# Optimization experiments

Hardware: AMD Instinct MI355X
Metric: run time of the kernel (lower is better)

The kernel has to match this reference:

```python
import jax, jax.numpy as jnp
import numpy as np

V, D, S, H, B = 32000, 1024, 2048, 16, 4
DFF = 4 * D
HD = D // H
EPS = 1e-5


def _layernorm(x, g, b):
    mu = jnp.mean(x, axis=-1, keepdims=True)
    var = jnp.var(x, axis=-1, keepdims=True)
    return (x - mu) * jax.lax.rsqrt(var + EPS) * g + b


def setup_inputs() -> dict:
    key = jax.random.key(0)
    ks = jax.random.split(key, 14)
    s = 0.02
    return {
        "tokens": jax.random.randint(ks[0], (B, S), 0, V),
        "emb": jax.random.normal(ks[1], (V, D), jnp.float32) * s,
        "pos": jax.random.normal(ks[2], (1, S, D), jnp.float32) * s,
        "w_qkv": jax.random.normal(ks[3], (3 * D, D), jnp.float32) * s,
        "b_qkv": jnp.zeros((3 * D,), jnp.float32),
        "w_o": jax.random.normal(ks[4], (D, D), jnp.float32) * s,
        "b_o": jnp.zeros((D,), jnp.float32),
        "g1": jnp.ones((D,), jnp.float32),
        "beta1": jnp.zeros((D,), jnp.float32),
        "w1": jax.random.normal(ks[5], (DFF, D), jnp.float32) * s,
        "b1": jnp.zeros((DFF,), jnp.float32),
        "w2": jax.random.normal(ks[6], (D, DFF), jnp.float32) * s,
        "b2": jnp.zeros((D,), jnp.float32),
        "g2": jnp.ones((D,), jnp.float32),
        "beta2": jnp.zeros((D,), jnp.float32),
        "w_fc": jax.random.normal(ks[7], (V, D), jnp.float32) * s,
        "b_fc": jnp.zeros((V,), jnp.float32),
    }


def reference(tokens, emb, pos, w_qkv, b_qkv, w_o, b_o, g1, beta1, w1, b1,
              w2, b2, g2, beta2, w_fc, b_fc):
    # embedding + learned positional embedding: [B, S, D]
    x = emb[tokens] + pos
    # multi-head self-attention (torch nn.MultiheadAttention semantics)
    qkv = jnp.einsum('bsd,ed->bse', x, w_qkv) + b_qkv
    q, k, v = jnp.split(qkv, 3, axis=-1)
    q = q.reshape(B, S, H, HD)
    k = k.reshape(B, S, H, HD)
    v = v.reshape(B, S, H, HD)
    scores = jnp.einsum('bqhd,bkhd->bhqk', q, k) / jnp.sqrt(jnp.float32(HD))
    attn = jax.nn.softmax(scores, axis=-1)
    ctx = jnp.einsum('bhqk,bkhd->bqhd', attn, v).reshape(B, S, D)
    attn_out = jnp.einsum('bsd,ed->bse', ctx, w_o) + b_o
    # residual + norm1
    x = _layernorm(x + attn_out, g1, beta1)
    # FFN with ReLU (the custom_relu is mathematically plain ReLU)
    h = jnp.maximum(jnp.einsum('bsd,fd->bsf', x, w1) + b1, 0.0)
    ffn = jnp.einsum('bsf,df->bsd', h, w2) + b2
    # residual + norm2
    x = _layernorm(x + ffn, g2, beta2)
    # final vocab projection
    logits = jnp.einsum('bsd,vd->bsv', x, w_fc) + b_fc
    return logits
```

## Files before the change

### kernel.cpp

```cpp
#include <hip/hip_runtime.h>
#include <stdint.h>

#define Bz   4
#define Sq   2048
#define Dm   1024
#define Hh   16
#define HDm  64
#define DFFm 4096
#define Vv   32000
#define MTOK (Bz * Sq)

typedef unsigned short u16;
typedef __attribute__((ext_vector_type(8))) short short8v;
typedef __attribute__((ext_vector_type(4))) float f32x4;

struct alignas(8) U16x4 { u16 x, y, z, w; };

typedef const __attribute__((address_space(1))) void* gptr1_t;
typedef __attribute__((address_space(3))) void* lptr3_t;

__device__ __forceinline__ u16 f2bf(float f) {
    union { float f; unsigned u; } v; v.f = f;
    unsigned r = v.u + 0x7FFF + ((v.u >> 16) & 1);
    return (u16)(r >> 16);
}
__device__ __forceinline__ float bf2f(u16 h) {
    union { unsigned u; float f; } v; v.u = ((unsigned)h) << 16;
    return v.f;
}

#define WAITVM(N) asm volatile("s_waitcnt vmcnt(" #N ")" ::: "memory")

__device__ __forceinline__ void barrier_fenced() {
    asm volatile("" ::: "memory");
    __builtin_amdgcn_s_barrier();
    asm volatile("" ::: "memory");
}

__global__ void to_bf16(const float* __restrict__ in, u16* __restrict__ out, long n4) {
    long i = (long)blockIdx.x * blockDim.x + threadIdx.x;
    const long stride = (long)gridDim.x * blockDim.x;
    for (; i < n4; i += stride) {
        float4 v = *(const float4*)(in + i * 4);
        U16x4 h = { f2bf(v.x), f2bf(v.y), f2bf(v.z), f2bf(v.w) };
        *(U16x4*)(out + i * 4) = h;
    }
}

__global__ void embed_kernel(const int* __restrict__ tok, const float* __restrict__ emb,
                             const float* __restrict__ pos, float* __restrict__ x32,
                             u16* __restrict__ x16) {
    const int row = blockIdx.x;
    const int s = row & (Sq - 1);
    const int t = threadIdx.x;
    const long tokid = tok[row];
    float4 e = *(const float4*)(emb + tokid * Dm + t * 4);
    float4 p = *(const float4*)(pos + (long)s * Dm + t * 4);
    float4 v = { e.x + p.x, e.y + p.y, e.z + p.z, e.w + p.w };
    const long base = (long)row * Dm + t * 4;
    *(float4*)(x32 + base) = v;
    U16x4 h = { f2bf(v.x), f2bf(v.y), f2bf(v.z), f2bf(v.w) };
    *(U16x4*)(x16 + base) = h;
}

template <int OUTMODE, int RELU>
__global__ __launch_bounds__(512, 2) void gemm256(
    const u16* __restrict__ A, const u16* __restrict__ B,
    const float* __restrict__ bias, void* __restrict__ Cp,
    int M, int N, int K, float alpha)
{
    __shared__ u16 smem[81920];

    const int bid = blockIdx.x;
    const int mtiles = M >> 8;
    const int mpx = mtiles >> 3;
    const int x   = bid & 7;
    const int loc = bid >> 3;
    const int im  = x * mpx + (loc % mpx);
    const int in  = loc / mpx;
    const int row0 = im * 256, col0 = in * 256;

    const int t = threadIdx.x;
    const int lane = t & 63;
    const int wid = t >> 6;
    const int wm = (wid >> 1) * 64;
    const int wn = (wid & 1) * 128;
    const int fr = lane & 15;
    const int g4 = lane >> 4;

    f32x4 acc[4][8];
#pragma unroll
    for (int m = 0; m < 4; ++m)
#pragma unroll
        for (int n = 0; n < 8; ++n) acc[m][n] = f32x4{0.f, 0.f, 0.f, 0.f};

    const int nt = K >> 6;
    const int srow = t >> 3;
    const int sc8  = t & 7;

    auto stage_half = [&](const u16* __restrict__ g, int rowbase, int h, u16* dst) {
#pragma unroll
        for (int j = 0; j < 2; ++j) {
            const int rl = h * 128 + srow + j * 64;
            const int c8 = sc8 ^ (rl & 7);
            const u16* sp = g + (long)(rowbase + rl) * K + c8 * 8;
            __builtin_amdgcn_global_load_lds((gptr1_t)sp,
                (lptr3_t)(dst + rl * 64 + sc8 * 8), 16, 0, 0);
        }
    };

    auto rdA = [&](const u16* base, int kk, int m) -> short8v {
        const int r = wm + m * 16 + fr;
        const int c8 = kk * 4 + g4;
        return *(const short8v*)(base + r * 64 + ((c8 ^ (r & 7)) << 3));
    };
    auto rdB = [&](const u16* base, int kk, int n) -> short8v {
        const int r = wn + n * 16 + fr;
        const int c8 = kk * 4 + g4;
        return *(const short8v*)(base + r * 64 + ((c8 ^ (r & 7)) << 3));
    };

    stage_half(A, row0, 0, smem);
    stage_half(A, row0, 1, smem);
    stage_half(B, col0, 0, smem + 32768);
    stage_half(B, col0, 1, smem + 32768);
    if (nt > 1) {
        stage_half(B + 64, col0, 0, smem + 49152);
        stage_half(B + 64, col0, 1, smem + 49152);
        WAITVM(4);
    } else {
        WAITVM(0);
    }
    barrier_fenced();

    short8v fa[4][2], fbl[4][2], fbh[4][2];

    for (int tt = 0; tt < nt; ++tt) {
        u16* rA = smem + ((tt & 1) << 14);
        u16* rB = smem + 32768 + ((unsigned)tt % 3u) * 16384;
        u16* sA = smem + ((~tt & 1) << 14);
        u16* sB = smem + 32768 + ((unsigned)(tt + 2) % 3u) * 16384;
        const bool stA = (tt + 1 < nt);
        const bool stB = (tt + 2 < nt);

#pragma unroll
        for (int m = 0; m < 4; ++m) fa[m][0] = rdA(rA, 0, m);
#pragma unroll
        for (int n = 0; n < 4; ++n) fbl[n][0] = rdB(rB, 0, n);
        if (stA) stage_half(A + (tt + 1) * 64, row0, 0, sA);
        barrier_fenced();
        asm volatile("s_waitcnt lgkmcnt(0)" ::: "memory");
        __builtin_amdgcn_s_setprio(1);
#pragma unroll
        for (int m = 0; m < 4; ++m)
#pragma unroll
            for (int n = 0; n < 4; ++n)
                acc[m][n] = __builtin_amdgcn_mfma_f32_16x16x32_bf16(fa[m][0], fbl[n][0], acc[m][n], 0, 0, 0);
        __builtin_amdgcn_s_setprio(0);
        barrier_fenced();

#pragma unroll
        for (int m = 0; m < 4; ++m) fa[m][1] = rdA(rA, 1, m);
#pragma unroll
        for (int n = 0; n < 4; ++n) fbl[n][1] = rdB(rB, 1, n);
        if (stA) stage_half(A + (tt + 1) * 64, row0, 1, sA);
        barrier_fenced();
        asm volatile("s_waitcnt lgkmcnt(0)" ::: "memory");
        __builtin_amdgcn_s_setprio(1);
#pragma unroll
        for (int m = 0; m < 4; ++m)
#pragma unroll
            for (int n = 0; n < 4; ++n)
                acc[m][n] = __builtin_amdgcn_mfma_f32_16x16x32_bf16(fa[m][1], fbl[n][1], acc[m][n], 0, 0, 0);
        __builtin_amdgcn_s_setprio(0);
        barrier_fenced();

#pragma unroll
        for (int n = 0; n < 4; ++n) fbh[n][0] = rdB(rB, 0, n + 4);
        if (stB) stage_half(B + (tt + 2) * 64, col0, 0, sB);
        barrier_fenced();
        asm volatile("s_waitcnt lgkmcnt(0)" ::: "memory");
        __builtin_amdgcn_s_setprio(1);
#pragma unroll
        for (int m = 0; m < 4; ++m)
#pragma unroll
            for (int n = 0; n < 4; ++n)
                acc[m][n + 4] = __builtin_amdgcn_mfma_f32_16x16x32_bf16(fa[m][0], fbh[n][0], acc[m][n + 4], 0, 0, 0);
        __builtin_amdgcn_s_setprio(0);
        barrier_fenced();

#pragma unroll
        for (int n = 0; n < 4; ++n) fbh[n][1] = rdB(rB, 1, n + 4);
        if (stB) stage_half(B + (tt + 2) * 64, col0, 1, sB);
        if (tt + 2 < nt) { WAITVM(4); } else { WAITVM(0); }
        barrier_fenced();
        asm volatile("s_waitcnt lgkmcnt(0)" ::: "memory");
        __builtin_amdgcn_s_setprio(1);
#pragma unroll
        for (int m = 0; m < 4; ++m)
#pragma unroll
            for (int n = 0; n < 4; ++n)
                acc[m][n + 4] = __builtin_amdgcn_mfma_f32_16x16x32_bf16(fa[m][1], fbh[n][1], acc[m][n + 4], 0, 0, 0);
        __builtin_amdgcn_s_setprio(0);
        barrier_fenced();
    }

    const int rq = (lane >> 4) * 4;
    float bv[8];
#pragma unroll
    for (int n = 0; n < 8; ++n)
        bv[n] = bias ? bias[col0 + wn + n * 16 + fr] : 0.f;
#pragma unroll
    for (int m = 0; m < 4; ++m) {
#pragma unroll
        for (int n = 0; n < 8; ++n) {
            const int col = col0 + wn + n * 16 + fr;
#pragma unroll
            for (int r = 0; r < 4; ++r) {
                const int row = row0 + wm + m * 16 + rq + r;
                float v = alpha * acc[m][n][r] + bv[n];
                if (RELU) v = fmaxf(v, 0.f);
                if (OUTMODE == 0)
                    ((float*)Cp)[(long)row * N + col] = v;
                else
                    ((u16*)Cp)[(long)row * N + col] = f2bf(v);
            }
        }
    }
}

__global__ void transpose_v(const u16* __restrict__ qkv, u16* __restrict__ vt) {
    const int kt = blockIdx.x * 64;
    const int bh = blockIdx.y;
    const int b = bh >> 4, h = bh & 15;
    const int t = threadIdx.x;
    __shared__ u16 tile[64][72];
    const long src = (long)b * Sq * (3 * Dm) + 2 * Dm + h * HDm;
#pragma unroll
    for (int i = 0; i < 2; ++i) {
        const int kl = i * 32 + (t >> 3);
        const int d0 = (t & 7) * 8;
        short8v v = *(const short8v*)(qkv + src + (long)(kt + kl) * (3 * Dm) + d0);
        *(short8v*)(&tile[kl][d0]) = v;
    }
    __syncthreads();
#pragma unroll
    for (int i = 0; i < 2; ++i) {
        const int d = i * 32 + (t >> 3);
        const int kk0 = (t & 7) * 8;
        short8v o;
#pragma unroll
        for (int j = 0; j < 8; ++j) o[j] = (short)tile[kk0 + j][d];
        *(short8v*)(vt + ((long)bh * HDm + d) * Sq + kt + kk0) = o;
    }
}

__global__ __launch_bounds__(256) void flash_attn(
    const u16* __restrict__ qkv, const u16* __restrict__ vt,
    u16* __restrict__ ctx)
{
    __shared__ u16 Kt[2][64 * 64];
    __shared__ u16 Vt[2][64 * 64];
    __shared__ u16 Pt[4][32 * 64];

    const int bh = blockIdx.y;
    const int b = bh >> 4, h = bh & 15;
    const int t = threadIdx.x;
    const int lane = t & 63;
    const int wid = t >> 6;
    const int fr = lane & 15;
    const int g = lane >> 4;
    const int qb = blockIdx.x * 128 + wid * 32;

    short8v aq[2][2];
#pragma unroll
    for (int qn = 0; qn < 2; ++qn)
#pragma unroll
        for (int kk = 0; kk < 2; ++kk) {
            const long q = (long)b * Sq + qb + qn * 16 + fr;
            aq[qn][kk] = *(const short8v*)(qkv + q * (3 * Dm) + h * 64 + kk * 32 + g * 8);
        }

    const int srl = t >> 3;
    const int sc8 = t & 7;
    const long kbase = (long)b * Sq * (3 * Dm) + Dm + h * 64;
    const long vbase = (long)bh * HDm * Sq;

    auto stage = [&](int kt, int buf) {
#pragma unroll
        for (int j = 0; j < 2; ++j) {
            const int rl = srl + j * 32;
            const int c8 = sc8 ^ (rl & 7);
            const u16* ks = qkv + kbase + (long)(kt * 64 + rl) * (3 * Dm) + c8 * 8;
            __builtin_amdgcn_global_load_lds((gptr1_t)ks,
                (lptr3_t)(&Kt[buf][rl * 64 + sc8 * 8]), 16, 0, 0);
            const u16* vs = vt + vbase + (long)rl * Sq + kt * 64 + c8 * 8;
            __builtin_amdgcn_global_load_lds((gptr1_t)vs,
                (lptr3_t)(&Vt[buf][rl * 64 + sc8 * 8]), 16, 0, 0);
        }
    };

    f32x4 accO[4][2];
#pragma unroll
    for (int dm = 0; dm < 4; ++dm)
#pragma unroll
        for (int qn = 0; qn < 2; ++qn) accO[dm][qn] = f32x4{0.f, 0.f, 0.f, 0.f};
    float m0 = -3.0e38f, m1 = -3.0e38f, l0 = 0.f, l1 = 0.f;
    const float cl2 = 0.125f * 1.44269504f;

    stage(0, 0);
    WAITVM(0);
    barrier_fenced();

    for (int kt = 0; kt < Sq / 64; ++kt) {
        const int cur = kt & 1;
        if (kt + 1 < Sq / 64) stage(kt + 1, cur ^ 1);

        f32x4 s[4][2];
#pragma unroll
        for (int kvm = 0; kvm < 4; ++kvm)
#pragma unroll
            for (int qn = 0; qn < 2; ++qn) s[kvm][qn] = f32x4{0.f, 0.f, 0.f, 0.f};
        __builtin_amdgcn_s_setprio(1);
#pragma unroll
        for (int kvm = 0; kvm < 4; ++kvm)
#pragma unroll
            for (int kk = 0; kk < 2; ++kk) {
                const int r = kvm * 16 + fr;
                short8v bk = *(const short8v*)(&Kt[cur][r * 64 + (((kk * 4 + g) ^ (r & 7)) << 3)]);
#pragma unroll
                for (int qn = 0; qn < 2; ++qn)
                    s[kvm][qn] = __builtin_amdgcn_mfma_f32_16x16x32_bf16(bk, aq[qn][kk], s[kvm][qn], 0, 0, 0);
            }
        __builtin_amdgcn_s_setprio(0);

        float t0 = -3.0e38f, t1 = -3.0e38f;
#pragma unroll
        for (int kvm = 0; kvm < 4; ++kvm)
#pragma unroll
            for (int r = 0; r < 4; ++r) {
                t0 = fmaxf(t0, s[kvm][0][r]);
                t1 = fmaxf(t1, s[kvm][1][r]);
            }
        t0 = fmaxf(t0, __shfl_xor(t0, 16)); t0 = fmaxf(t0, __shfl_xor(t0, 32));
        t1 = fmaxf(t1, __shfl_xor(t1, 16)); t1 = fmaxf(t1, __shfl_xor(t1, 32));
        const float mn0 = fmaxf(m0, t0 * cl2);
        const float mn1 = fmaxf(m1, t1 * cl2);
        const float a0 = __builtin_amdgcn_exp2f(m0 - mn0);
        const float a1 = __builtin_amdgcn_exp2f(m1 - mn1);
        m0 = mn0; m1 = mn1;

        float ps0 = 0.f, ps1 = 0.f;
#pragma unroll
        for (int kvm = 0; kvm < 4; ++kvm)
#pragma unroll
            for (int r = 0; r < 4; ++r) {
                float p0 = __builtin_amdgcn_exp2f(s[kvm][0][r] * cl2 - mn0);
                float p1 = __builtin_amdgcn_exp2f(s[kvm][1][r] * cl2 - mn1);
                s[kvm][0][r] = p0; ps0 += p0;
                s[kvm][1][r] = p1; ps1 += p1;
            }
        ps0 += __shfl_xor(ps0, 16); ps0 += __shfl_xor(ps0, 32);
        ps1 += __shfl_xor(ps1, 16); ps1 += __shfl_xor(ps1, 32);
        l0 = l0 * a0 + ps0;
        l1 = l1 * a1 + ps1;
#pragma unroll
        for (int dm = 0; dm < 4; ++dm)
#pragma unroll
            for (int r = 0; r < 4; ++r) {
                accO[dm][0][r] *= a0;
                accO[dm][1][r] *= a1;
            }

#pragma unroll
        for (int kvm = 0; kvm < 4; ++kvm)
#pragma unroll
            for (int qn = 0; qn < 2; ++qn) {
                U16x4 hh = { f2bf(s[kvm][qn][0]), f2bf(s[kvm][qn][1]),
                             f2bf(s[kvm][qn][2]), f2bf(s[kvm][qn][3]) };
                const int q = qn * 16 + fr;
                const int off = q * 64 + (((2 * kvm + (g >> 1)) ^ (fr & 7)) << 3) + (g & 1) * 4;
                *(U16x4*)(&Pt[wid][off]) = hh;
            }
        short8v pb[2][2];
        short8v va[4][2];
#pragma unroll
        for (int qn = 0; qn < 2; ++qn)
#pragma unroll
            for (int ks = 0; ks < 2; ++ks) {
                const int q = qn * 16 + fr;
                pb[qn][ks] = *(const short8v*)(&Pt[wid][q * 64 + (((ks * 4 + g) ^ (fr & 7)) << 3)]);
            }
#pragma unroll
        for (int dm = 0; dm < 4; ++dm)
#pragma unroll
            for (int ks = 0; ks < 2; ++ks) {
                const int r = dm * 16 + fr;
                va[dm][ks] = *(const short8v*)(&Vt[cur][r * 64 + (((ks * 4 + g) ^ (r & 7)) << 3)]);
            }

        __builtin_amdgcn_s_setprio(1);
#pragma unroll
        for (int dm = 0; dm < 4; ++dm)
#pragma unroll
            for (int qn = 0; qn < 2; ++qn)
#pragma unroll
                for (int ks = 0; ks < 2; ++ks)
                    accO[dm][qn] = __builtin_amdgcn_mfma_f32_16x16x32_bf16(va[dm][ks], pb[qn][ks], accO[dm][qn], 0, 0, 0);
        __builtin_amdgcn_s_setprio(0);

        WAITVM(0);
        barrier_fenced();
    }

    const float inv0 = 1.f / l0;
    const float inv1 = 1.f / l1;
#pragma unroll
    for (int dm = 0; dm < 4; ++dm)
#pragma unroll
        for (int qn = 0; qn < 2; ++qn) {
            const float inv = qn ? inv1 : inv0;
            U16x4 hh = { f2bf(accO[dm][qn][0] * inv), f2bf(accO[dm][qn][1] * inv),
                         f2bf(accO[dm][qn][2] * inv), f2bf(accO[dm][qn][3] * inv) };
            const long q = (long)b * Sq + qb + qn * 16 + fr;
            *(U16x4*)(ctx + q * Dm + h * 64 + dm * 16 + g * 4) = hh;
        }
}

template <int W32>
__global__ void ln_kernel(float* __restrict__ x, const float* __restrict__ res,
                          const float* __restrict__ g, const float* __restrict__ be,
                          u16* __restrict__ out16) {
    const int row = blockIdx.x;
    const int t = threadIdx.x;
    const long base = (long)row * Dm + t * 4;
    float4 a = *(const float4*)(x + base);
    float4 b = *(const float4*)(res + base);
    float v0 = a.x + b.x, v1 = a.y + b.y, v2 = a.z + b.z, v3 = a.w + b.w;
    float s = v0 + v1 + v2 + v3;
    float q = v0 * v0 + v1 * v1 + v2 * v2 + v3 * v3;

    const int wave = t >> 6, lane = t & 63;
    __shared__ float rs[4], rq2[4];
#pragma unroll
    for (int o = 32; o; o >>= 1) { s += __shfl_xor(s, o); q += __shfl_xor(q, o); }
    if (lane == 0) { rs[wave] = s; rq2[wave] = q; }
    __syncthreads();
    s = rs[0] + rs[1] + rs[2] + rs[3];
    q = rq2[0] + rq2[1] + rq2[2] + rq2[3];

    const float mean = s * (1.f / Dm);
    const float var = q * (1.f / Dm) - mean * mean;
    const float rstd = rsqrtf(var + 1e-5f);
    const float4 gg = *(const float4*)(g + t * 4);
    const float4 bb = *(const float4*)(be + t * 4);
    float o0 = (v0 - mean) * rstd * gg.x + bb.x;
    float o1 = (v1 - mean) * rstd * gg.y + bb.y;
    float o2 = (v2 - mean) * rstd * gg.z + bb.z;
    float o3 = (v3 - mean) * rstd * gg.w + bb.w;
    U16x4 h = { f2bf(o0), f2bf(o1), f2bf(o2), f2bf(o3) };
    *(U16x4*)(out16 + base) = h;
    if (W32) {
        float4 ov = { o0, o1, o2, o3 };
        *(float4*)(x + base) = ov;
    }
}

extern "C" void kernel_launch(void* const* d_in, const int* in_sizes, int n_in,
                              void* d_out, int out_size, void* d_ws, size_t ws_size,
                              hipStream_t stream) {
    const int*   tokens = (const int*)  d_in[0];
    const float* emb    = (const float*)d_in[1];
    const float* pos    = (const float*)d_in[2];
    const float* w_qkv  = (const float*)d_in[3];
    const float* b_qkv  = (const float*)d_in[4];
    const float* w_o    = (const float*)d_in[5];
    const float* b_o    = (const float*)d_in[6];
    const float* g1     = (const float*)d_in[7];
    const float* beta1  = (const float*)d_in[8];
    const float* w1     = (const float*)d_in[9];
    const float* b1     = (const float*)d_in[10];
    const float* w2     = (const float*)d_in[11];
    const float* b2     = (const float*)d_in[12];
    const float* g2     = (const float*)d_in[13];
    const float* beta2  = (const float*)d_in[14];
    const float* w_fc   = (const float*)d_in[15];
    const float* b_fc   = (const float*)d_in[16];

    char* ws = (char*)d_ws;
    size_t off = 0;
    auto alloc = [&](size_t bytes) { void* p = ws + off; off += (bytes + 255) & ~(size_t)255; return p; };

    float* X32   = (float*)alloc((size_t)MTOK * Dm * 4);
    u16*   XB16  = (u16*)  alloc((size_t)MTOK * Dm * 2);
    u16*   QKV16 = (u16*)  alloc((size_t)MTOK * 3 * Dm * 2);
    u16*   VT16  = (u16*)  alloc((size_t)64 * HDm * Sq * 2);
    u16*   CTX16 = (u16*)  alloc((size_t)MTOK * Dm * 2);
    float* ATT32 = (float*)alloc((size_t)MTOK * Dm * 4);
    u16*   H16   = (u16*)  alloc((size_t)MTOK * DFFm * 2);
    u16*   WQ16  = (u16*)  alloc((size_t)3 * Dm * Dm * 2);
    u16*   WO16  = (u16*)  alloc((size_t)Dm * Dm * 2);
    u16*   W116  = (u16*)  alloc((size_t)DFFm * Dm * 2);
    u16*   W216  = (u16*)  alloc((size_t)Dm * DFFm * 2);
    u16*   WFC16 = (u16*)  alloc((size_t)Vv * Dm * 2);

    const dim3 blk(256);
    const dim3 blk512(512);

    to_bf16<<<1024, blk, 0, stream>>>(w_qkv, WQ16, (long)3 * Dm * Dm / 4);
    to_bf16<<<1024, blk, 0, stream>>>(w_o,   WO16, (long)Dm * Dm / 4);
    to_bf16<<<1024, blk, 0, stream>>>(w1,    W116, (long)DFFm * Dm / 4);
    to_bf16<<<1024, blk, 0, stream>>>(w2,    W216, (long)Dm * DFFm / 4);
    to_bf16<<<2048, blk, 0, stream>>>(w_fc,  WFC16, (long)Vv * Dm / 4);

    embed_kernel<<<MTOK, blk, 0, stream>>>(tokens, emb, pos, X32, XB16);

    gemm256<1, 0><<<dim3((MTOK / 256) * ((3 * Dm) / 256)), blk512, 0, stream>>>(
        XB16, WQ16, b_qkv, QKV16, MTOK, 3 * Dm, Dm, 1.f);

    transpose_v<<<dim3(Sq / 64, Bz * Hh), blk, 0, stream>>>(QKV16, VT16);

    flash_attn<<<dim3(Sq / 128, Bz * Hh), blk, 0, stream>>>(QKV16, VT16, CTX16);

    gemm256<0, 0><<<dim3((MTOK / 256) * (Dm / 256)), blk512, 0, stream>>>(
        CTX16, WO16, b_o, ATT32, MTOK, Dm, Dm, 1.f);

    ln_kernel<1><<<MTOK, blk, 0, stream>>>(X32, ATT32, g1, beta1, XB16);

    gemm256<1, 1><<<dim3((MTOK / 256) * (DFFm / 256)), blk512, 0, stream>>>(
        XB16, W116, b1, H16, MTOK, DFFm, Dm, 1.f);

    gemm256<0, 0><<<dim3((MTOK / 256) * (Dm / 256)), blk512, 0, stream>>>(
        H16, W216, b2, ATT32, MTOK, Dm, DFFm, 1.f);

    ln_kernel<0><<<MTOK, blk, 0, stream>>>(X32, ATT32, g2, beta2, XB16);

    gemm256<0, 0><<<dim3((MTOK / 256) * (Vv / 256)), blk512, 0, stream>>>(
        XB16, WFC16, b_fc, (float*)d_out, MTOK, Vv, Dm, 1.f);
}
```

Before: 1.165 ms.

## Replace 256x256 GEMM tile with 128x128 tile and 3-stage K pipeline

Swaps the 512-thread 256x256 GEMM kernel for a 256-thread 128x128 kernel with K=32 steps and a three-stage shared-memory ring for both operands, using a new XOR swizzle. Smaller tiles use far less LDS and allow more blocks in flight for better occupancy and simpler scheduling. In exchange, each loaded byte feeds fewer MFMAs and there are more barriers per FLOP, which can raise memory traffic on these large GEMMs.

New measurement: 1.282 ms. 1.1x slower.

```diff
diff --git a/kernel.cpp b/kernel.cpp
--- a/kernel.cpp
+++ b/kernel.cpp
@@ -64,90 +64,86 @@
 }
 
 template <int OUTMODE, int RELU>
-__global__ __launch_bounds__(512, 2) void gemm256(
+__global__ __launch_bounds__(256) void gemm128(
     const u16* __restrict__ A, const u16* __restrict__ B,
     const float* __restrict__ bias, void* __restrict__ Cp,
     int M, int N, int K, float alpha)
 {
-    __shared__ u16 smem[81920];
+    __shared__ u16 smem[24576];
 
     const int bid = blockIdx.x;
-    const int mtiles = M >> 8;
+    const int mtiles = M >> 7;
     const int mpx = mtiles >> 3;
     const int x   = bid & 7;
     const int loc = bid >> 3;
     const int im  = x * mpx + (loc % mpx);
     const int in  = loc / mpx;
-    const int row0 = im * 256, col0 = in * 256;
+    const int row0 = im * 128, col0 = in * 128;
 
     const int t = threadIdx.x;
     const int lane = t & 63;
     const int wid = t >> 6;
-    const int wm = (wid >> 1) * 64;
-    const int wn = (wid & 1) * 128;
+    const int wr = (wid >> 1) * 64;
+    const int wc = (wid & 1) * 64;
     const int fr = lane & 15;
     const int g4 = lane >> 4;
 
-    f32x4 acc[4][8];
+    f32x4 acc[4][4];
 #pragma unroll
     for (int m = 0; m < 4; ++m)
 #pragma unroll
-        for (int n = 0; n < 8; ++n) acc[m][n] = f32x4{0.f, 0.f, 0.f, 0.f};
-
-    const int nt = K >> 6;
-    const int srow = t >> 3;
-    const int sc8  = t & 7;
-
-    auto stage_half = [&](const u16* __restrict__ g, int rowbase, int h, u16* dst) {
+        for (int n = 0; n < 4; ++n) acc[m][n] = f32x4{0.f, 0.f, 0.f, 0.f};
+
+    const int nt = K >> 5;
+
+    auto stage = [&](const u16* __restrict__ g, int rowbase, u16* dst) {
 #pragma unroll
         for (int j = 0; j < 2; ++j) {
-            const int rl = h * 128 + srow + j * 64;
-            const int c8 = sc8 ^ (rl & 7);
-            const u16* sp = g + (long)(rowbase + rl) * K + c8 * 8;
+            const int slot = j * 256 + t;
+            const int row = slot >> 2;
+            const int c8 = (slot & 3) ^ ((row >> 1) & 3);
+            const u16* sp = g + (long)(rowbase + row) * K + c8 * 8;
             __builtin_amdgcn_global_load_lds((gptr1_t)sp,
-                (lptr3_t)(dst + rl * 64 + sc8 * 8), 16, 0, 0);
+                (lptr3_t)(dst + slot * 8), 16, 0, 0);
         }
     };
 
-    auto rdA = [&](const u16* base, int kk, int m) -> short8v {
-        const int r = wm + m * 16 + fr;
-        const int c8 = kk * 4 + g4;
-        return *(const short8v*)(base + r * 64 + ((c8 ^ (r & 7)) << 3));
+    auto rdT = [&](const u16* base, int rbase) -> short8v {
+        const int r = rbase + fr;
+        return *(const short8v*)(base + r * 32 + ((g4 ^ ((r >> 1) & 3)) << 3));
     };
-    auto rdB = [&](const u16* base, int kk, int n) -> short8v {
-        const int r = wn + n * 16 + fr;
-        const int c8 = kk * 4 + g4;
-        return *(const short8v*)(base + r * 64 + ((c8 ^ (r & 7)) << 3));
-    };
-
-    stage_half(A, row0, 0, smem);
-    stage_half(A, row0, 1, smem);
-    stage_half(B, col0, 0, smem + 32768);
-    stage_half(B, col0, 1, smem + 32768);
+
+    stage(A, row0, smem);
+    stage(B, col0, smem + 12288);
     if (nt > 1) {
-        stage_half(B + 64, col0, 0, smem + 49152);
-        stage_half(B + 64, col0, 1, smem + 49152);
+        stage(A + 32, row0, smem + 4096);
+        stage(B + 32, col0, smem + 12288 + 4096);
         WAITVM(4);
     } else {
         WAITVM(0);
     }
     barrier_fenced();
 
-    short8v fa[4][2], fbl[4][2], fbh[4][2];
+    short8v fa[4], fb[4];
 
     for (int tt = 0; tt < nt; ++tt) {
-        u16* rA = smem + ((tt & 1) << 14);
-        u16* rB = smem + 32768 + ((unsigned)tt % 3u) * 16384;
-        u16* sA = smem + ((~tt & 1) << 14);
-        u16* sB = smem + 32768 + ((unsigned)(tt + 2) % 3u) * 16384;
-        const bool stA = (tt + 1 < nt);
-        const bool stB = (tt + 2 < nt);
-
-#pragma unroll
-        for (int m = 0; m < 4; ++m) fa[m][0] = rdA(rA, 0, m);
-#pragma unroll
-        for (int n = 0; n < 4; ++n) fbl[n][0] = rdB(rB, 0, n);
-        if (stA) stage_half(A + (tt + 1) * 64, row0, 0, sA);
+        u16* rA = smem + ((unsigned)tt % 3u) * 4096;
+        u16* rB = smem + 12288 + ((unsigned)tt % 3u) * 4096;
+        u16* sA = smem + ((unsigned)(tt + 2) % 3u) * 4096;
+        u16* sB = smem + 12288 + ((unsigned)(tt + 2) % 3u) * 4096;
+
+#pragma unroll
+        for (int m = 0; m < 4; ++m) fa[m] = rdT(rA, wr + m * 16);
+#pragma unroll
+        for (int n = 0; n < 4; ++n) fb[n] = rdT(rB, wc + n * 16);
+
+        if (tt + 2 < nt) {
+            stage(A + (tt + 2) * 32, row0, sA);
+            stage(B + (tt + 2) * 32, col0, sB);
+            WAITVM(4);
+        } else {
+            WAITVM(0);
+        }
         barrier_fenced();
         asm volatile("s_waitcnt lgkmcnt(0)" ::: "memory");
         __builtin_amdgcn_s_setprio(1);
@@ -155,69 +151,24 @@
         for (int m = 0; m < 4; ++m)
 #pragma unroll
             for (int n = 0; n < 4; ++n)
-                acc[m][n] = __builtin_amdgcn_mfma_f32_16x16x32_bf16(fa[m][0], fbl[n][0], acc[m][n], 0, 0, 0);
+                acc[m][n] = __builtin_amdgcn_mfma_f32_16x16x32_bf16(fa[m], fb[n], acc[m][n], 0, 0, 0);
         __builtin_amdgcn_s_setprio(0);
         barrier_fenced();
-
-#pragma unroll
-        for (int m = 0; m < 4; ++m) fa[m][1] = rdA(rA, 1, m);
-#pragma unroll
-        for (int n = 0; n < 4; ++n) fbl[n][1] = rdB(rB, 1, n);
-        if (stA) stage_half(A + (tt + 1) * 64, row0, 1, sA);
-        barrier_fenced();
-        asm volatile("s_waitcnt lgkmcnt(0)" ::: "memory");
-        __builtin_amdgcn_s_setprio(1);
-#pragma unroll
-        for (int m = 0; m < 4; ++m)
-#pragma unroll
-            for (int n = 0; n < 4; ++n)
-                acc[m][n] = __builtin_amdgcn_mfma_f32_16x16x32_bf16(fa[m][1], fbl[n][1], acc[m][n], 0, 0, 0);
-        __builtin_amdgcn_s_setprio(0);
-        barrier_fenced();
-
-#pragma unroll
-        for (int n = 0; n < 4; ++n) fbh[n][0] = rdB(rB, 0, n + 4);
-        if (stB) stage_half(B + (tt + 2) * 64, col0, 0, sB);
-        barrier_fenced();
-        asm volatile("s_waitcnt lgkmcnt(0)" ::: "memory");
-        __builtin_amdgcn_s_setprio(1);
-#pragma unroll
-        for (int m = 0; m < 4; ++m)
-#pragma unroll
-            for (int n = 0; n < 4; ++n)
-                acc[m][n + 4] = __builtin_amdgcn_mfma_f32_16x16x32_bf16(fa[m][0], fbh[n][0], acc[m][n + 4], 0, 0, 0);
-        __builtin_amdgcn_s_setprio(0);
-        barrier_fenced();
-
-#pragma unroll
-        for (int n = 0; n < 4; ++n) fbh[n][1] = rdB(rB, 1, n + 4);
-        if (stB) stage_half(B + (tt + 2) * 64, col0, 1, sB);
-        if (tt + 2 < nt) { WAITVM(4); } else { WAITVM(0); }
-        barrier_fenced();
-        asm volatile("s_waitcnt lgkmcnt(0)" ::: "memory");
-        __builtin_amdgcn_s_setprio(1);
-#pragma unroll
-        for (int m = 0; m < 4; ++m)
-#pragma unroll
-            for (int n = 0; n < 4; ++n)
-                acc[m][n + 4] = __builtin_amdgcn_mfma_f32_16x16x32_bf16(fa[m][1], fbh[n][1], acc[m][n + 4], 0, 0, 0);
-        __builtin_amdgcn_s_setprio(0);
-        barrier_fenced();
     }
 
     const int rq = (lane >> 4) * 4;
-    float bv[8];
-#pragma unroll
-    for (int n = 0; n < 8; ++n)
-        bv[n] = bias ? bias[col0 + wn + n * 16 + fr] : 0.f;
+    float bv[4];
+#pragma unroll
+    for (int n = 0; n < 4; ++n)
+        bv[n] = bias ? bias[col0 + wc + n * 16 + fr] : 0.f;
 #pragma unroll
     for (int m = 0; m < 4; ++m) {
 #pragma unroll
-        for (int n = 0; n < 8; ++n) {
-            const int col = col0 + wn + n * 16 + fr;
+        for (int n = 0; n < 4; ++n) {
+            const int col = col0 + wc + n * 16 + fr;
 #pragma unroll
             for (int r = 0; r < 4; ++r) {
-                const int row = row0 + wm + m * 16 + rq + r;
+                const int row = row0 + wr + m * 16 + rq + r;
                 float v = alpha * acc[m][n][r] + bv[n];
                 if (RELU) v = fmaxf(v, 0.f);
                 if (OUTMODE == 0)
@@ -505,7 +456,6 @@
     u16*   WFC16 = (u16*)  alloc((size_t)Vv * Dm * 2);
 
     const dim3 blk(256);
-    const dim3 blk512(512);
 
     to_bf16<<<1024, blk, 0, stream>>>(w_qkv, WQ16, (long)3 * Dm * Dm / 4);
     to_bf16<<<1024, blk, 0, stream>>>(w_o,   WO16, (long)Dm * Dm / 4);
@@ -515,26 +465,26 @@
 
     embed_kernel<<<MTOK, blk, 0, stream>>>(tokens, emb, pos, X32, XB16);
 
-    gemm256<1, 0><<<dim3((MTOK / 256) * ((3 * Dm) / 256)), blk512, 0, stream>>>(
+    gemm128<1, 0><<<dim3((MTOK / 128) * ((3 * Dm) / 128)), blk, 0, stream>>>(
         XB16, WQ16, b_qkv, QKV16, MTOK, 3 * Dm, Dm, 1.f);
 
     transpose_v<<<dim3(Sq / 64, Bz * Hh), blk, 0, stream>>>(QKV16, VT16);
 
     flash_attn<<<dim3(Sq / 128, Bz * Hh), blk, 0, stream>>>(QKV16, VT16, CTX16);
 
-    gemm256<0, 0><<<dim3((MTOK / 256) * (Dm / 256)), blk512, 0, stream>>>(
+    gemm128<0, 0><<<dim3((MTOK / 128) * (Dm / 128)), blk, 0, stream>>>(
         CTX16, WO16, b_o, ATT32, MTOK, Dm, Dm, 1.f);
 
     ln_kernel<1><<<MTOK, blk, 0, stream>>>(X32, ATT32, g1, beta1, XB16);
 
-    gemm256<1, 1><<<dim3((MTOK / 256) * (DFFm / 256)), blk512, 0, stream>>>(
+    gemm128<1, 1><<<dim3((MTOK / 128) * (DFFm / 128)), blk, 0, stream>>>(
         XB16, W116, b1, H16, MTOK, DFFm, Dm, 1.f);
 
-    gemm256<0, 0><<<dim3((MTOK / 256) * (Dm / 256)), blk512, 0, stream>>>(
+    gemm128<0, 0><<<dim3((MTOK / 128) * (Dm / 128)), blk, 0, stream>>>(
         H16, W216, b2, ATT32, MTOK, Dm, DFFm, 1.f);
 
     ln_kernel<0><<<MTOK, blk, 0, stream>>>(X32, ATT32, g2, beta2, XB16);
 
-    gemm256<0, 0><<<dim3((MTOK / 256) * (Vv / 256)), blk512, 0, stream>>>(
+    gemm128<0, 0><<<dim3((MTOK / 128) * (Vv / 128)), blk, 0, stream>>>(
         XB16, WFC16, b_fc, (float*)d_out, MTOK, Vv, Dm, 1.f);
 }
```

## Add 128x256 triple-buffered GEMM kernel for vocab projection

Applied to the files above, without the earlier changes.

Adds a new gemm_tb kernel with 256 threads and 128x256 output tiles, K-step 32, a three-stage LDS ring fed by global_load_lds, and swizzled shared-memory reads. Block indices are remapped into eight groups of M-tiles to improve L2 locality. It replaces the 512-thread 256x256 GEMM only for the final vocab logits projection. Smaller tiles double the block count and may improve occupancy and load balance, at the cost of less reuse per loaded tile.

Result: slower. 1.467 ms (+25.9%).

```diff
diff --git a/kernel.cpp b/kernel.cpp
--- a/kernel.cpp
+++ b/kernel.cpp
@@ -201,6 +201,127 @@
 #pragma unroll
             for (int n = 0; n < 4; ++n)
                 acc[m][n + 4] = __builtin_amdgcn_mfma_f32_16x16x32_bf16(fa[m][1], fbh[n][1], acc[m][n + 4], 0, 0, 0);
+        __builtin_amdgcn_s_setprio(0);
+        barrier_fenced();
+    }
+
+    const int rq = (lane >> 4) * 4;
+    float bv[8];
+#pragma unroll
+    for (int n = 0; n < 8; ++n)
+        bv[n] = bias ? bias[col0 + wn + n * 16 + fr] : 0.f;
+#pragma unroll
+    for (int m = 0; m < 4; ++m) {
+#pragma unroll
+        for (int n = 0; n < 8; ++n) {
+            const int col = col0 + wn + n * 16 + fr;
+#pragma unroll
+            for (int r = 0; r < 4; ++r) {
+                const int row = row0 + wm + m * 16 + rq + r;
+                float v = alpha * acc[m][n][r] + bv[n];
+                if (RELU) v = fmaxf(v, 0.f);
+                if (OUTMODE == 0)
+                    ((float*)Cp)[(long)row * N + col] = v;
+                else
+                    ((u16*)Cp)[(long)row * N + col] = f2bf(v);
+            }
+        }
+    }
+}
+
+template <int OUTMODE, int RELU>
+__global__ __launch_bounds__(256) void gemm_tb(
+    const u16* __restrict__ A, const u16* __restrict__ B,
+    const float* __restrict__ bias, void* __restrict__ Cp,
+    int M, int N, int K, float alpha)
+{
+    __shared__ u16 smem[36864];
+
+    const int bid = blockIdx.x;
+    const int mtiles = M >> 7;
+    const int mpx = mtiles >> 3;
+    const int x   = bid & 7;
+    const int loc = bid >> 3;
+    const int im  = x * mpx + (loc % mpx);
+    const int in  = loc / mpx;
+    const int row0 = im * 128, col0 = in * 256;
+
+    const int t = threadIdx.x;
+    const int lane = t & 63;
+    const int wid = t >> 6;
+    const int wm = (wid >> 1) * 64;
+    const int wn = (wid & 1) * 128;
+    const int fr = lane & 15;
+    const int g4 = lane >> 4;
+
+    f32x4 acc[4][8];
+#pragma unroll
+    for (int m = 0; m < 4; ++m)
+#pragma unroll
+        for (int n = 0; n < 8; ++n) acc[m][n] = f32x4{0.f, 0.f, 0.f, 0.f};
+
+    const int nt = K >> 5;
+
+    auto stageA = [&](const u16* __restrict__ g, u16* dst) {
+#pragma unroll
+        for (int j = 0; j < 2; ++j) {
+            const int slot = j * 256 + t;
+            const int row = slot >> 2;
+            const int c4 = (slot & 3) ^ ((row >> 1) & 3);
+            const u16* sp = g + (long)(row0 + row) * K + c4 * 8;
+            __builtin_amdgcn_global_load_lds((gptr1_t)sp,
+                (lptr3_t)(dst + slot * 8), 16, 0, 0);
+        }
+    };
+    auto stageB = [&](const u16* __restrict__ g, u16* dst) {
+#pragma unroll
+        for (int j = 0; j < 4; ++j) {
+            const int slot = j * 256 + t;
+            const int row = slot >> 2;
+            const int c4 = (slot & 3) ^ ((row >> 1) & 3);
+            const u16* sp = g + (long)(col0 + row) * K + c4 * 8;
+            __builtin_amdgcn_global_load_lds((gptr1_t)sp,
+                (lptr3_t)(dst + slot * 8), 16, 0, 0);
+        }
+    };
+
+    auto rdT = [&](const u16* base, int rbase) -> short8v {
+        const int r = rbase + fr;
+        return *(const short8v*)(base + r * 32 + ((g4 ^ ((r >> 1) & 3)) << 3));
+    };
+
+    stageA(A, smem);
+    stageB(B, smem + 12288);
+    WAITVM(0);
+    stageA(A + 32, smem + 4096);
+    stageB(B + 32, smem + 12288 + 8192);
+    barrier_fenced();
+
+    for (int tt = 0; tt < nt; ++tt) {
+        u16* rA = smem + ((unsigned)tt % 3u) * 4096;
+        u16* rB = smem + 12288 + ((unsigned)tt % 3u) * 8192;
+
+        short8v fa[4], fb[8];
+#pragma unroll
+        for (int m = 0; m < 4; ++m) fa[m] = rdT(rA, wm + m * 16);
+#pragma unroll
+        for (int n = 0; n < 8; ++n) fb[n] = rdT(rB, wn + n * 16);
+
+        if (tt + 2 < nt) {
+            stageA(A + (tt + 2) * 32, smem + ((unsigned)(tt + 2) % 3u) * 4096);
+            stageB(B + (tt + 2) * 32, smem + 12288 + ((unsigned)(tt + 2) % 3u) * 8192);
+            WAITVM(6);
+        } else {
+            WAITVM(0);
+        }
+        barrier_fenced();
+        asm volatile("s_waitcnt lgkmcnt(0)" ::: "memory");
+        __builtin_amdgcn_s_setprio(1);
+#pragma unroll
+        for (int m = 0; m < 4; ++m)
+#pragma unroll
+            for (int n = 0; n < 8; ++n)
+                acc[m][n] = __builtin_amdgcn_mfma_f32_16x16x32_bf16(fa[m], fb[n], acc[m][n], 0, 0, 0);
         __builtin_amdgcn_s_setprio(0);
         barrier_fenced();
     }
@@ -535,6 +656,6 @@
 
     ln_kernel<0><<<MTOK, blk, 0, stream>>>(X32, ATT32, g2, beta2, XB16);
 
-    gemm256<0, 0><<<dim3((MTOK / 256) * (Vv / 256)), blk512, 0, stream>>>(
+    gemm_tb<0, 0><<<dim3((MTOK / 128) * (Vv / 256)), blk, 0, stream>>>(
         XB16, WFC16, b_fc, (float*)d_out, MTOK, Vv, Dm, 1.f);
 }
```
